# Kernel optimization log

Measured on AMD Instinct MI355X. Metric: run time of the kernel, lower is better.

The kernel has to match this reference:

```python
import jax, jax.numpy as jnp
import numpy as np

KH = KW = 3
K = KH * KW
GROUPS = 8


def conv_same(x, w, b=None):
    out = jax.lax.conv_general_dilated(x, w, (1, 1), 'SAME',
                                       dimension_numbers=('NHWC', 'HWIO', 'NHWC'))
    if b is not None:
        out = out + b
    return out


def feature_selection(x, w_att, w_sel):
    pooled = x.mean(axis=(1, 2), keepdims=True)            # [B,1,1,C]
    attn = jax.nn.sigmoid(conv_same(pooled, w_att))        # 1x1 conv, sigmoid
    return conv_same(x * (attn + 1.0), w_sel)              # [B,H,W,F]


def deform_sample(x, sy, sx):
    # x: [H,W,G,Cg]; sy,sx: [H,W,G,K] fractional sample coords (zero outside)
    H, W, G, _ = x.shape
    y0 = jnp.floor(sy)
    x0 = jnp.floor(sx)
    wy1 = sy - y0
    wx1 = sx - x0
    gi = jnp.arange(G)[None, None, :, None]

    def gather(yi, xi):
        valid = (yi >= 0) & (yi <= H - 1) & (xi >= 0) & (xi <= W - 1)
        yc = jnp.clip(yi, 0, H - 1).astype(jnp.int32)
        xc = jnp.clip(xi, 0, W - 1).astype(jnp.int32)
        v = x[yc, xc, gi]                                   # [H,W,G,K,Cg]
        return v * valid[..., None]

    v00 = gather(y0, x0)
    v01 = gather(y0, x0 + 1)
    v10 = gather(y0 + 1, x0)
    v11 = gather(y0 + 1, x0 + 1)
    wy1 = wy1[..., None]
    wx1 = wx1[..., None]
    top = v00 * (1 - wx1) + v01 * wx1
    bot = v10 * (1 - wx1) + v11 * wx1
    return top * (1 - wy1) + bot * wy1                      # [H,W,G,K,Cg]


def dcnv2(x, align, w_om, b_om, w_dcn, b_dcn):
    # x: [B,H,W,C] input to deform-conv; align: [B,H,W,Ca] alignment feature
    B, H, W, C = x.shape
    G = GROUPS
    Cg = C // G
    om = conv_same(align, w_om, b_om)                       # [B,H,W,G*3*K]
    off = om[..., :G * 2 * K].reshape(B, H, W, G, K, 2)     # (dy, dx)
    mask = jax.nn.sigmoid(om[..., G * 2 * K:]).reshape(B, H, W, G, K)

    iy = jnp.arange(H, dtype=x.dtype)[:, None, None, None]
    ix = jnp.arange(W, dtype=x.dtype)[None, :, None, None]
    ky, kx = jnp.meshgrid(jnp.arange(KH) - (KH - 1) // 2,
                          jnp.arange(KW) - (KW - 1) // 2, indexing='ij')
    ky = ky.reshape(K).astype(x.dtype)
    kx = kx.reshape(K).astype(x.dtype)
    sy = iy + ky + off[..., 0]                              # [B,H,W,G,K]
    sx = ix + kx + off[..., 1]

    xg = x.reshape(B, H, W, G, Cg)
    sampled = jax.vmap(deform_sample)(xg, sy, sx)           # [B,H,W,G,K,Cg]
    sampled = sampled * mask[..., None]
    sampled = sampled.transpose(0, 1, 2, 4, 3, 5).reshape(B, H, W, K, C)
    wk = w_dcn.reshape(K, C, -1)                            # [K,C,F]
    return jnp.einsum('bhwkc,kcf->bhwf', sampled, wk) + b_dcn


def reference(coarse, fine, w_att, w_sel, w_off, w_om, b_om, w_dcn, b_dcn):
    B, H, W, _ = fine.shape
    coarse_up = jax.image.resize(coarse, (B, H, W, coarse.shape[-1]), 'bilinear')
    fine_cal = feature_selection(fine, w_att, w_sel)
    fc = jnp.concatenate([fine_cal, coarse_up * 2.0], axis=-1)
    align = conv_same(fc, w_off)                            # 1x1, no bias
    aligned = jax.nn.relu(dcnv2(coarse_up, align, w_om, b_om, w_dcn, b_dcn))
    return aligned + fine_cal


def setup_inputs() -> dict:
    key = jax.random.key(0)
    ks = jax.random.split(key, 8)
    B, H, W = 4, 64, 64
    Cc, Cf, F = 256, 256, 256
    s = lambda fan: (2.0 / fan) ** 0.5
    return {
        'coarse': jax.random.normal(ks[0], (B, H // 2, W // 2, Cc), jnp.float32),
        'fine': jax.random.normal(ks[1], (B, H, W, Cf), jnp.float32),
        'w_att': jax.random.normal(ks[2], (1, 1, Cf, Cf), jnp.float32) * s(Cf),
        'w_sel': jax.random.normal(ks[3], (1, 1, Cf, F), jnp.float32) * s(Cf),
        'w_off': jax.random.normal(ks[4], (1, 1, F + Cc, 2 * F), jnp.float32) * s(F + Cc),
        'w_om': jax.random.normal(ks[5], (3, 3, 2 * F, GROUPS * 3 * K), jnp.float32) * 0.01,
        'b_om': jnp.zeros((GROUPS * 3 * K,), jnp.float32),
        'w_dcn': jax.random.normal(ks[6], (3, 3, Cc, F), jnp.float32) * s(9 * Cc),
        'b_dcn': jnp.zeros((F,), jnp.float32),
    }
```

## Files before the change

kernel.cpp:

```cpp
#include <hip/hip_runtime.h>
#include <hip/hip_bf16.h>
#include <cstddef>

constexpr int HWP = 64 * 64;
constexpr int CCH = 256;
constexpr int OMC = 216;
constexpr int KDC = 2304;

typedef __attribute__((ext_vector_type(8))) short bf16x8;
typedef __attribute__((ext_vector_type(4))) float f32x4;

__device__ inline unsigned short f2bf(float x) {
  __hip_bfloat16 h = __float2bfloat16(x);
  return *reinterpret_cast<unsigned short*>(&h);
}
__device__ inline float bf2f(unsigned short u) {
  unsigned int v = ((unsigned int)u) << 16;
  return __uint_as_float(v);
}
__device__ inline void bfpair(unsigned int u, float& a, float& b) {
  a = __uint_as_float(u << 16);
  b = __uint_as_float(u & 0xffff0000u);
}

__global__ __launch_bounds__(256) void prep_weights(
    const float* __restrict__ w_off, const float* __restrict__ w_om,
    const float* __restrict__ w_sel, const float* __restrict__ w_dcn,
    unsigned short* __restrict__ w_offT, unsigned short* __restrict__ w_omT,
    unsigned short* __restrict__ w_selT, unsigned short* __restrict__ w_dcnT) {
  int i = blockIdx.x * 256 + threadIdx.x;
  if (i < 512 * 512) {
    int n = i >> 9, k = i & 511;
    w_offT[i] = f2bf(w_off[k * 512 + n]);
  }
  if (i < 9 * 256 * 512) {
    int c = i & 511;
    int r = i >> 9;
    int tap = r >> 8;
    int n = r & 255;
    w_omT[i] = f2bf(n < OMC ? w_om[((size_t)tap * 512 + c) * OMC + n] : 0.f);
  }
  if (i < 256 * 256) {
    int n = i >> 8, k = i & 255;
    w_selT[i] = f2bf(w_sel[k * 256 + n]);
  }
  if (i < 9 * 256 * 256) {
    int tap = i >> 16, f = (i >> 8) & 255, c = i & 255;
    w_dcnT[i] = f2bf(w_dcn[((size_t)tap * 256 + c) * 256 + f]);
  }
}

__global__ __launch_bounds__(256) void pool_partial(
    const float* __restrict__ fine, float* __restrict__ partial) {
  int r = blockIdx.x;
  int b = blockIdx.y;
  int t = threadIdx.x;
  const float* src = fine + ((size_t)b * 4096 + r * 64) * 256 + t;
  float s = 0.f;
#pragma unroll 8
  for (int p = 0; p < 64; ++p) s += src[(size_t)p * 256];
  partial[((size_t)b * 64 + r) * 256 + t] = s;
}

__global__ __launch_bounds__(256) void pool_finish(
    const float* __restrict__ partial, const float* __restrict__ w_att,
    float* __restrict__ scale) {
  __shared__ float pl[256];
  int b = blockIdx.x;
  int t = threadIdx.x;
  const float* pp = partial + (size_t)b * 64 * 256 + t;
  float s = 0.f;
#pragma unroll 8
  for (int r = 0; r < 64; ++r) s += pp[(size_t)r * 256];
  pl[t] = s * (1.0f / 4096.0f);
  __syncthreads();
  float acc = 0.f;
  for (int ci = 0; ci < 256; ++ci) acc += pl[ci] * w_att[ci * 256 + t];
  scale[b * 256 + t] = 1.0f + 1.0f / (1.0f + expf(-acc));
}

__global__ __launch_bounds__(256) void upsample_kernel(
    const float* __restrict__ coarse, unsigned short* __restrict__ upbf,
    unsigned short* __restrict__ alignA) {
  int m = blockIdx.x;
  int c = threadIdx.x;
  int b = m >> 12, h = (m >> 6) & 63, w = m & 63;
  float cy = fminf(fmaxf(h * 0.5f - 0.25f, 0.f), 31.f);
  float cx = fminf(fmaxf(w * 0.5f - 0.25f, 0.f), 31.f);
  int y0 = (int)cy, x0 = (int)cx;
  float fy = cy - y0, fx = cx - x0;
  int y1 = min(y0 + 1, 31), x1 = min(x0 + 1, 31);
  const float* base = coarse + (size_t)b * 32 * 32 * CCH;
  float v00 = base[(y0 * 32 + x0) * CCH + c];
  float v01 = base[(y0 * 32 + x1) * CCH + c];
  float v10 = base[(y1 * 32 + x0) * CCH + c];
  float v11 = base[(y1 * 32 + x1) * CCH + c];
  float top = v00 + (v01 - v00) * fx;
  float bot = v10 + (v11 - v10) * fx;
  float v = top + (bot - top) * fy;
  upbf[(size_t)m * CCH + c] = f2bf(v);
  alignA[(size_t)m * 512 + 256 + c] = f2bf(2.f * v);
}

__global__ __launch_bounds__(256) void gemm_finecal_mfma(
    const float* __restrict__ fine, const float* __restrict__ scale,
    const unsigned short* __restrict__ w_selT,
    float* __restrict__ finecal, unsigned short* __restrict__ alignA) {
  __shared__ unsigned short As[128][72];
  __shared__ unsigned short Bs[64][72];
  __shared__ float sc[256];
  int n0 = blockIdx.x * 64;
  int m0 = blockIdx.y * 128;
  int t = threadIdx.x;
  int wid = t >> 6, lane = t & 63;
  int lrow = lane & 15, lq = lane >> 4;
  int bb = m0 >> 12;
  sc[t] = scale[bb * 256 + t];
  f32x4 acc[2][4];
#pragma unroll
  for (int i = 0; i < 2; ++i)
#pragma unroll
    for (int j = 0; j < 4; ++j) acc[i][j] = (f32x4){0.f, 0.f, 0.f, 0.f};
  for (int k0 = 0; k0 < 256; k0 += 64) {
    __syncthreads();
    for (int u = t; u < 128 * 8; u += 256) {
      int row = u >> 3, ck = u & 7;
      const float* fp = &fine[(size_t)(m0 + row) * 256 + k0 + ck * 8];
      float4 f0 = *(const float4*)fp;
      float4 f1 = *(const float4*)(fp + 4);
      int kb = k0 + ck * 8;
      ushort4 u0 = make_ushort4(f2bf(f0.x * sc[kb]), f2bf(f0.y * sc[kb + 1]),
                                f2bf(f0.z * sc[kb + 2]), f2bf(f0.w * sc[kb + 3]));
      ushort4 u1 = make_ushort4(f2bf(f1.x * sc[kb + 4]), f2bf(f1.y * sc[kb + 5]),
                                f2bf(f1.z * sc[kb + 6]), f2bf(f1.w * sc[kb + 7]));
      *(ushort4*)&As[row][ck * 8] = u0;
      *(ushort4*)&As[row][ck * 8 + 4] = u1;
    }
    for (int u = t; u < 64 * 8; u += 256) {
      int row = u >> 3, ck = u & 7;
      *(uint4*)&Bs[row][ck * 8] = *(const uint4*)&w_selT[(size_t)(n0 + row) * 256 + k0 + ck * 8];
    }
    __syncthreads();
#pragma unroll
    for (int kk = 0; kk < 2; ++kk) {
      bf16x8 a[2], b[4];
#pragma unroll
      for (int mt = 0; mt < 2; ++mt)
        a[mt] = *(const bf16x8*)&As[wid * 32 + mt * 16 + lrow][kk * 32 + lq * 8];
#pragma unroll
      for (int nt = 0; nt < 4; ++nt)
        b[nt] = *(const bf16x8*)&Bs[nt * 16 + lrow][kk * 32 + lq * 8];
#pragma unroll
      for (int mt = 0; mt < 2; ++mt)
#pragma unroll
        for (int nt = 0; nt < 4; ++nt)
          acc[mt][nt] = __builtin_amdgcn_mfma_f32_16x16x32_bf16(
              a[mt], b[nt], acc[mt][nt], 0, 0, 0);
    }
  }
#pragma unroll
  for (int mt = 0; mt < 2; ++mt)
#pragma unroll
    for (int nt = 0; nt < 4; ++nt)
#pragma unroll
      for (int r = 0; r < 4; ++r) {
        int m = m0 + wid * 32 + mt * 16 + lq * 4 + r;
        int n = n0 + nt * 16 + lrow;
        finecal[(size_t)m * 256 + n] = acc[mt][nt][r];
        alignA[(size_t)m * 512 + n] = f2bf(acc[mt][nt][r]);
      }
}

__global__ __launch_bounds__(256) void gemm_align_mfma(
    const unsigned short* __restrict__ alignA,
    const unsigned short* __restrict__ w_offT,
    unsigned short* __restrict__ alignBf) {
  __shared__ unsigned short As[128][72];
  __shared__ unsigned short Bs[64][72];
  int n0 = blockIdx.x * 64;
  int m0 = blockIdx.y * 128;
  int t = threadIdx.x;
  int wid = t >> 6, lane = t & 63;
  int lrow = lane & 15, lq = lane >> 4;
  f32x4 acc[2][4];
#pragma unroll
  for (int i = 0; i < 2; ++i)
#pragma unroll
    for (int j = 0; j < 4; ++j) acc[i][j] = (f32x4){0.f, 0.f, 0.f, 0.f};
  for (int k0 = 0; k0 < 512; k0 += 64) {
    __syncthreads();
    for (int u = t; u < 128 * 8; u += 256) {
      int row = u >> 3, ck = u & 7;
      *(uint4*)&As[row][ck * 8] =
          *(const uint4*)&alignA[(size_t)(m0 + row) * 512 + k0 + ck * 8];
    }
    for (int u = t; u < 64 * 8; u += 256) {
      int row = u >> 3, ck = u & 7;
      *(uint4*)&Bs[row][ck * 8] =
          *(const uint4*)&w_offT[(size_t)(n0 + row) * 512 + k0 + ck * 8];
    }
    __syncthreads();
#pragma unroll
    for (int kk = 0; kk < 2; ++kk) {
      bf16x8 a[2], b[4];
#pragma unroll
      for (int mt = 0; mt < 2; ++mt)
        a[mt] = *(const bf16x8*)&As[wid * 32 + mt * 16 + lrow][kk * 32 + lq * 8];
#pragma unroll
      for (int nt = 0; nt < 4; ++nt)
        b[nt] = *(const bf16x8*)&Bs[nt * 16 + lrow][kk * 32 + lq * 8];
#pragma unroll
      for (int mt = 0; mt < 2; ++mt)
#pragma unroll
        for (int nt = 0; nt < 4; ++nt)
          acc[mt][nt] = __builtin_amdgcn_mfma_f32_16x16x32_bf16(
              a[mt], b[nt], acc[mt][nt], 0, 0, 0);
    }
  }
#pragma unroll
  for (int mt = 0; mt < 2; ++mt)
#pragma unroll
    for (int nt = 0; nt < 4; ++nt)
#pragma unroll
      for (int r = 0; r < 4; ++r) {
        int m = m0 + wid * 32 + mt * 16 + lq * 4 + r;
        int n = n0 + nt * 16 + lrow;
        alignBf[(size_t)m * 512 + n] = f2bf(acc[mt][nt][r]);
      }
}

__global__ __launch_bounds__(256) void om_conv_mfma(
    const unsigned short* __restrict__ alignBf,
    const unsigned short* __restrict__ w_omT,
    const float* __restrict__ b_om,
    float* __restrict__ om) {
  __shared__ unsigned short As[4][66][72];
  __shared__ unsigned short Bs[2][64][72];
  int nblk = blockIdx.x;
  int mblk = blockIdx.y;
  int b = mblk >> 5, hp = mblk & 31;
  int h0 = hp * 2;
  int n0 = nblk * 64;
  int t = threadIdx.x;
  int wid = t >> 6, lane = t & 63;
  int wy = wid >> 1, wx = wid & 1;
  int lrow = lane & 15, lq = lane >> 4;
  const size_t imgbase = (size_t)b * 4096;
  f32x4 acc[4][2];
#pragma unroll
  for (int i = 0; i < 4; ++i)
#pragma unroll
    for (int j = 0; j < 2; ++j) acc[i][j] = (f32x4){0.f, 0.f, 0.f, 0.f};

  auto stageB = [&](int buf, int tap, int c0) {
    for (int u = t; u < 64 * 8; u += 256) {
      int n = u >> 3, ck = u & 7;
      *(uint4*)&Bs[buf][n][ck * 8] =
          *(const uint4*)&w_omT[((size_t)tap * 256 + n0 + n) * 512 + c0 * 64 + ck * 8];
    }
  };
  auto stageA = [&](int c0) {
    for (int u = t; u < 4 * 66 * 8; u += 256) {
      int dy = u / 528;
      int r = u - dy * 528;
      int px = r >> 3, ck = r & 7;
      int w = px - 1;
      int y = h0 - 1 + dy;
      uint4 v = make_uint4(0u, 0u, 0u, 0u);
      if (w >= 0 && w < 64 && y >= 0 && y < 64)
        v = *(const uint4*)&alignBf[(imgbase + y * 64 + w) * 512 + c0 * 64 + ck * 8];
      *(uint4*)&As[dy][px][ck * 8] = v;
    }
  };

  stageB(0, 0, 0);
  stageA(0);
  __syncthreads();
  int buf = 0;
  for (int c0 = 0; c0 < 8; ++c0) {
    for (int tap = 0; tap < 9; ++tap) {
      int ntap = tap + 1, nc0 = c0;
      if (ntap == 9) { ntap = 0; nc0 = (c0 + 1) & 7; }
      stageB(buf ^ 1, ntap, nc0);
      int dyt = tap / 3, dxt = tap - dyt * 3;
#pragma unroll
      for (int kk = 0; kk < 2; ++kk) {
        bf16x8 a[4], bb[2];
#pragma unroll
        for (int mt = 0; mt < 4; ++mt)
          a[mt] = *(const bf16x8*)&As[wy + dyt][mt * 16 + lrow + dxt][kk * 32 + lq * 8];
#pragma unroll
        for (int nt = 0; nt < 2; ++nt)
          bb[nt] = *(const bf16x8*)&Bs[buf][wx * 32 + nt * 16 + lrow][kk * 32 + lq * 8];
#pragma unroll
        for (int mt = 0; mt < 4; ++mt)
#pragma unroll
          for (int nt = 0; nt < 2; ++nt)
            acc[mt][nt] = __builtin_amdgcn_mfma_f32_16x16x32_bf16(
                a[mt], bb[nt], acc[mt][nt], 0, 0, 0);
      }
      __syncthreads();
      buf ^= 1;
    }
    if (c0 < 7) {
      stageA(c0 + 1);
      __syncthreads();
    }
  }
#pragma unroll
  for (int nt = 0; nt < 2; ++nt) {
    int n = n0 + wx * 32 + nt * 16 + lrow;
    if (n < OMC) {
      float bias = b_om[n];
#pragma unroll
      for (int mt = 0; mt < 4; ++mt) {
#pragma unroll
        for (int r = 0; r < 4; ++r) {
          size_t m = imgbase + (size_t)(h0 + wy) * 64 + mt * 16 + lq * 4 + r;
          om[m * OMC + n] = acc[mt][nt][r] + bias;
        }
      }
    }
  }
}

__global__ __launch_bounds__(256) void dcn_sample(
    const float* __restrict__ om, const unsigned short* __restrict__ upbf,
    unsigned short* __restrict__ S, int bh0) {
  __shared__ int offsA[256][4];
  __shared__ float wtsA[256][4];
  int blk = blockIdx.x;
  int bh = bh0 + (blk >> 1);
  int half = blk & 1;
  int b = bh >> 6, h = bh & 63;
  int p0 = half * 32;
  int m0g = bh * 64 + p0;
  int mloc0 = (bh - bh0) * 64 + p0;
  int t = threadIdx.x;
  const unsigned short* upb = upbf + (size_t)b * HWP * CCH;
  int lane = t & 63;
  int ph = t >> 6;
  int c = lane * 4;
  int g = lane >> 3;
  for (int tap = 0; tap < 9; ++tap) {
    int ky = tap / 3, kx = tap - ky * 3;
    __syncthreads();
    {
      int p = t >> 3, gg = t & 7;
      const float* omr = om + (size_t)(m0g + p) * OMC;
      float dy = omr[gg * 18 + tap * 2];
      float dx = omr[gg * 18 + tap * 2 + 1];
      float mk = 1.0f / (1.0f + expf(-omr[144 + gg * 9 + tap]));
      float sy = (float)(h + ky - 1) + dy;
      float sx = (float)(p0 + p + kx - 1) + dx;
      float y0f = floorf(sy), x0f = floorf(sx);
      float fy = sy - y0f, fx = sx - x0f;
      int y0 = (int)y0f, x0 = (int)x0f;
      int y1 = y0 + 1, x1 = x0 + 1;
      float vy0 = (y0 >= 0 && y0 <= 63) ? 1.f : 0.f;
      float vy1 = (y1 >= 0 && y1 <= 63) ? 1.f : 0.f;
      float vx0 = (x0 >= 0 && x0 <= 63) ? 1.f : 0.f;
      float vx1 = (x1 >= 0 && x1 <= 63) ? 1.f : 0.f;
      int yc0 = min(max(y0, 0), 63), yc1 = min(max(y1, 0), 63);
      int xc0 = min(max(x0, 0), 63), xc1 = min(max(x1, 0), 63);
      offsA[t][0] = (yc0 * 64 + xc0) * 256;
      offsA[t][1] = (yc0 * 64 + xc1) * 256;
      offsA[t][2] = (yc1 * 64 + xc0) * 256;
      offsA[t][3] = (yc1 * 64 + xc1) * 256;
      wtsA[t][0] = (1.f - fy) * (1.f - fx) * vy0 * vx0 * mk;
      wtsA[t][1] = (1.f - fy) * fx * vy0 * vx1 * mk;
      wtsA[t][2] = fy * (1.f - fx) * vy1 * vx0 * mk;
      wtsA[t][3] = fy * fx * vy1 * vx1 * mk;
    }
    __syncthreads();
#pragma unroll
    for (int pp = 0; pp < 8; ++pp) {
      int p = ph * 8 + pp;
      int idx = (p << 3) | g;
      int4 o = *(const int4*)&offsA[idx][0];
      float4 wv = *(const float4*)&wtsA[idx][0];
      uint2 u00 = *(const uint2*)&upb[o.x + c];
      uint2 u01 = *(const uint2*)&upb[o.y + c];
      uint2 u10 = *(const uint2*)&upb[o.z + c];
      uint2 u11 = *(const uint2*)&upb[o.w + c];
      float a0, a1, a2, a3, b0, b1, b2, b3, c0, c1, c2, c3, d0, d1, d2, d3;
      bfpair(u00.x, a0, a1); bfpair(u00.y, a2, a3);
      bfpair(u01.x, b0, b1); bfpair(u01.y, b2, b3);
      bfpair(u10.x, c0, c1); bfpair(u10.y, c2, c3);
      bfpair(u11.x, d0, d1); bfpair(u11.y, d2, d3);
      float v0 = wv.x * a0 + wv.y * b0 + wv.z * c0 + wv.w * d0;
      float v1 = wv.x * a1 + wv.y * b1 + wv.z * c1 + wv.w * d1;
      float v2 = wv.x * a2 + wv.y * b2 + wv.z * c2 + wv.w * d2;
      float v3 = wv.x * a3 + wv.y * b3 + wv.z * c3 + wv.w * d3;
      uint2 outv;
      outv.x = (unsigned int)f2bf(v0) | ((unsigned int)f2bf(v1) << 16);
      outv.y = (unsigned int)f2bf(v2) | ((unsigned int)f2bf(v3) << 16);
      *(uint2*)&S[(size_t)(mloc0 + p) * KDC + tap * 256 + c] = outv;
    }
  }
}

__global__ __launch_bounds__(256) void dcn_gemm(
    const unsigned short* __restrict__ S,
    const unsigned short* __restrict__ w_dcnT,
    const float* __restrict__ b_dcn,
    const float* __restrict__ finecal,
    float* __restrict__ outp, int m_base, int kiters) {
  __shared__ unsigned short As[2][128][72];
  __shared__ unsigned short Bs[2][128][72];
  int n0 = blockIdx.x * 128;
  int mloc0 = blockIdx.y * 128;
  int m0 = m_base + mloc0;
  int t = threadIdx.x;
  int wid = t >> 6, lane = t & 63;
  int wy = wid >> 1, wx = wid & 1;
  int lrow = lane & 15, lq = lane >> 4;
  f32x4 acc[4][4];
#pragma unroll
  for (int i = 0; i < 4; ++i)
#pragma unroll
    for (int j = 0; j < 4; ++j) acc[i][j] = (f32x4){0.f, 0.f, 0.f, 0.f};

  int arow = t >> 3, ack = t & 7;
  uint4 pa[4], pb[4];
  auto loadA = [&](int k0, uint4* p) {
#pragma unroll
    for (int i = 0; i < 4; ++i)
      p[i] = *(const uint4*)&S[(size_t)(mloc0 + arow + i * 32) * KDC + k0 + ack * 8];
  };
  auto loadB = [&](int k0, uint4* p) {
    int tap = k0 >> 8, c0 = k0 & 255;
#pragma unroll
    for (int i = 0; i < 4; ++i)
      p[i] = *(const uint4*)&w_dcnT[((size_t)tap * 256 + n0 + arow + i * 32) * 256 + c0 + ack * 8];
  };
  auto storeTiles = [&](int buf, const uint4* a, const uint4* b) {
#pragma unroll
    for (int i = 0; i < 4; ++i)
      *(uint4*)&As[buf][arow + i * 32][ack * 8] = a[i];
#pragma unroll
    for (int i = 0; i < 4; ++i)
      *(uint4*)&Bs[buf][arow + i * 32][ack * 8] = b[i];
  };

  loadA(0, pa);
  loadB(0, pb);
  storeTiles(0, pa, pb);
  __syncthreads();
  int buf = 0;
  for (int kb = 0; kb < kiters; ++kb) {
    bool has_next = (kb + 1) < kiters;
    if (has_next) {
      loadA((kb + 1) * 64, pa);
      loadB((kb + 1) * 64, pb);
    }
#pragma unroll
    for (int kk = 0; kk < 2; ++kk) {
      bf16x8 a[4], b[4];
#pragma unroll
      for (int mt = 0; mt < 4; ++mt)
        a[mt] = *(const bf16x8*)&As[buf][wy * 64 + mt * 16 + lrow][kk * 32 + lq * 8];
#pragma unroll
      for (int nt = 0; nt < 4; ++nt)
        b[nt] = *(const bf16x8*)&Bs[buf][wx * 64 + nt * 16 + lrow][kk * 32 + lq * 8];
#pragma unroll
      for (int mt = 0; mt < 4; ++mt)
#pragma unroll
        for (int nt = 0; nt < 4; ++nt)
          acc[mt][nt] = __builtin_amdgcn_mfma_f32_16x16x32_bf16(
              a[mt], b[nt], acc[mt][nt], 0, 0, 0);
    }
    if (has_next) {
      storeTiles(buf ^ 1, pa, pb);
      __syncthreads();
      buf ^= 1;
    }
  }
#pragma unroll
  for (int mt = 0; mt < 4; ++mt)
#pragma unroll
    for (int nt = 0; nt < 4; ++nt) {
      int f = n0 + wx * 64 + nt * 16 + lrow;
      float bias = b_dcn[f];
#pragma unroll
      for (int r = 0; r < 4; ++r) {
        int m = m0 + wy * 64 + mt * 16 + lq * 4 + r;
        float v = fmaxf(acc[mt][nt][r] + bias, 0.f);
        float fc = __builtin_nontemporal_load(&finecal[(size_t)m * 256 + f]);
        __builtin_nontemporal_store(v + fc, &outp[(size_t)m * 256 + f]);
      }
    }
}

extern "C" void kernel_launch(void* const* d_in, const int* in_sizes, int n_in,
                              void* d_out, int out_size, void* d_ws, size_t ws_size,
                              hipStream_t stream) {
  const float* coarse = (const float*)d_in[0];
  const float* fine   = (const float*)d_in[1];
  const float* w_att  = (const float*)d_in[2];
  const float* w_sel  = (const float*)d_in[3];
  const float* w_off  = (const float*)d_in[4];
  const float* w_om   = (const float*)d_in[5];
  const float* b_om   = (const float*)d_in[6];
  const float* w_dcn  = (const float*)d_in[7];
  const float* b_dcn  = (const float*)d_in[8];
  float* outp = (float*)d_out;

  char* base = (char*)d_ws;
  size_t o = 0;
  float* scale            = (float*)(base + o);          o += 4096;
  float* finecal          = (float*)(base + o);          o += 16777216;
  float* omb              = (float*)(base + o);          o += 14155776;
  unsigned short* upbf    = (unsigned short*)(base + o); o += 8388608;
  unsigned short* w_offT  = (unsigned short*)(base + o); o += 524288;
  unsigned short* w_omT   = (unsigned short*)(base + o); o += 2359296;
  unsigned short* w_selT  = (unsigned short*)(base + o); o += 131072;
  unsigned short* w_dcnT  = (unsigned short*)(base + o); o += 1179648;
  unsigned short* Sbuf    = (unsigned short*)(base + o);
  size_t fixed = o;
  unsigned short* alignA  = Sbuf;
  unsigned short* alignBf = (unsigned short*)((char*)Sbuf + 16777216);
  float* partial = omb;

  bool fullS = (ws_size >= fixed + 75497472);

  prep_weights<<<dim3(4608), dim3(256), 0, stream>>>(
      w_off, w_om, w_sel, w_dcn, w_offT, w_omT, w_selT, w_dcnT);
  pool_partial<<<dim3(64, 4), dim3(256), 0, stream>>>(fine, partial);
  pool_finish<<<dim3(4), dim3(256), 0, stream>>>(partial, w_att, scale);
  upsample_kernel<<<dim3(16384), dim3(256), 0, stream>>>(coarse, upbf, alignA);
  gemm_finecal_mfma<<<dim3(4, 128), dim3(256), 0, stream>>>(
      fine, scale, w_selT, finecal, alignA);
  gemm_align_mfma<<<dim3(8, 128), dim3(256), 0, stream>>>(alignA, w_offT, alignBf);
  om_conv_mfma<<<dim3(4, 128), dim3(256), 0, stream>>>(alignBf, w_omT, b_om, omb);

  if (fullS) {
    dcn_sample<<<dim3(512), dim3(256), 0, stream>>>(omb, upbf, Sbuf, 0);
    dcn_gemm<<<dim3(2, 128), dim3(256), 0, stream>>>(
        Sbuf, w_dcnT, b_dcn, finecal, outp, 0, KDC / 64);
  } else {
    for (int ch = 0; ch < 2; ++ch) {
      dcn_sample<<<dim3(256), dim3(256), 0, stream>>>(omb, upbf, Sbuf, ch * 128);
      dcn_gemm<<<dim3(2, 64), dim3(256), 0, stream>>>(
          Sbuf, w_dcnT, b_dcn, finecal, outp, ch * 8192, KDC / 64);
    }
  }
}
```

Before: 424.0 us.

## Widen om_conv N tile to 128 and prefetch weights through registers

The offset/mask 3x3 conv kernel now computes 128 output channels per block instead of 64. That halves the grid and halves how often each block re-stages the same input tile from alignBf. Weight tiles for the next tap are loaded into registers before the MFMA work and written to shared memory afterwards, so global load latency overlaps compute. The cost is more accumulator registers and LDS per block, a smaller grid that may occupy the GPU less fully, and wasted MFMAs on padded channels beyond 216.

Result: slower. 451.3 us (+6.4%).

```diff
diff --git a/kernel.cpp b/kernel.cpp
--- a/kernel.cpp
+++ b/kernel.cpp
@@ -235,29 +235,35 @@
     const float* __restrict__ b_om,
     float* __restrict__ om) {
   __shared__ unsigned short As[4][66][72];
-  __shared__ unsigned short Bs[2][64][72];
+  __shared__ unsigned short Bs[2][128][72];
   int nblk = blockIdx.x;
   int mblk = blockIdx.y;
   int b = mblk >> 5, hp = mblk & 31;
   int h0 = hp * 2;
-  int n0 = nblk * 64;
+  int n0 = nblk * 128;
   int t = threadIdx.x;
   int wid = t >> 6, lane = t & 63;
   int wy = wid >> 1, wx = wid & 1;
   int lrow = lane & 15, lq = lane >> 4;
   const size_t imgbase = (size_t)b * 4096;
-  f32x4 acc[4][2];
+  f32x4 acc[4][4];
 #pragma unroll
   for (int i = 0; i < 4; ++i)
 #pragma unroll
-    for (int j = 0; j < 2; ++j) acc[i][j] = (f32x4){0.f, 0.f, 0.f, 0.f};
-
-  auto stageB = [&](int buf, int tap, int c0) {
-    for (int u = t; u < 64 * 8; u += 256) {
-      int n = u >> 3, ck = u & 7;
-      *(uint4*)&Bs[buf][n][ck * 8] =
-          *(const uint4*)&w_omT[((size_t)tap * 256 + n0 + n) * 512 + c0 * 64 + ck * 8];
-    }
+    for (int j = 0; j < 4; ++j) acc[i][j] = (f32x4){0.f, 0.f, 0.f, 0.f};
+
+  int brow = t >> 3, bck = t & 7;
+  uint4 pb[4];
+  auto loadB = [&](int tap, int c0, uint4* p) {
+#pragma unroll
+    for (int i = 0; i < 4; ++i)
+      p[i] = *(const uint4*)&w_omT[((size_t)tap * 256 + n0 + brow + i * 32) * 512 +
+                                   c0 * 64 + bck * 8];
+  };
+  auto storeB = [&](int buf, const uint4* p) {
+#pragma unroll
+    for (int i = 0; i < 4; ++i)
+      *(uint4*)&Bs[buf][brow + i * 32][bck * 8] = p[i];
   };
   auto stageA = [&](int c0) {
     for (int u = t; u < 4 * 66 * 8; u += 256) {
@@ -273,43 +279,48 @@
     }
   };
 
-  stageB(0, 0, 0);
+  loadB(0, 0, pb);
+  storeB(0, pb);
   stageA(0);
   __syncthreads();
   int buf = 0;
   for (int c0 = 0; c0 < 8; ++c0) {
     for (int tap = 0; tap < 9; ++tap) {
       int ntap = tap + 1, nc0 = c0;
-      if (ntap == 9) { ntap = 0; nc0 = (c0 + 1) & 7; }
-      stageB(buf ^ 1, ntap, nc0);
+      bool has_next = true;
+      if (ntap == 9) { ntap = 0; nc0 = c0 + 1; has_next = (nc0 < 8); }
+      if (has_next) loadB(ntap, nc0, pb);
       int dyt = tap / 3, dxt = tap - dyt * 3;
 #pragma unroll
       for (int kk = 0; kk < 2; ++kk) {
-        bf16x8 a[4], bb[2];
+        bf16x8 a[4], bb[4];
 #pragma unroll
         for (int mt = 0; mt < 4; ++mt)
           a[mt] = *(const bf16x8*)&As[wy + dyt][mt * 16 + lrow + dxt][kk * 32 + lq * 8];
 #pragma unroll
-        for (int nt = 0; nt < 2; ++nt)
-          bb[nt] = *(const bf16x8*)&Bs[buf][wx * 32 + nt * 16 + lrow][kk * 32 + lq * 8];
+        for (int nt = 0; nt < 4; ++nt)
+          bb[nt] = *(const bf16x8*)&Bs[buf][wx * 64 + nt * 16 + lrow][kk * 32 + lq * 8];
 #pragma unroll
         for (int mt = 0; mt < 4; ++mt)
 #pragma unroll
-          for (int nt = 0; nt < 2; ++nt)
+          for (int nt = 0; nt < 4; ++nt)
             acc[mt][nt] = __builtin_amdgcn_mfma_f32_16x16x32_bf16(
                 a[mt], bb[nt], acc[mt][nt], 0, 0, 0);
       }
-      __syncthreads();
-      buf ^= 1;
-    }
-    if (c0 < 7) {
-      stageA(c0 + 1);
-      __syncthreads();
-    }
-  }
-#pragma unroll
-  for (int nt = 0; nt < 2; ++nt) {
-    int n = n0 + wx * 32 + nt * 16 + lrow;
+      if (has_next) {
+        storeB(buf ^ 1, pb);
+        __syncthreads();
+        buf ^= 1;
+        if (tap == 8) {
+          stageA(nc0);
+          __syncthreads();
+        }
+      }
+    }
+  }
+#pragma unroll
+  for (int nt = 0; nt < 4; ++nt) {
+    int n = n0 + wx * 64 + nt * 16 + lrow;
     if (n < OMC) {
       float bias = b_om[n];
 #pragma unroll
@@ -532,7 +543,7 @@
   gemm_finecal_mfma<<<dim3(4, 128), dim3(256), 0, stream>>>(
       fine, scale, w_selT, finecal, alignA);
   gemm_align_mfma<<<dim3(8, 128), dim3(256), 0, stream>>>(alignA, w_offT, alignBf);
-  om_conv_mfma<<<dim3(4, 128), dim3(256), 0, stream>>>(alignBf, w_omT, b_om, omb);
+  om_conv_mfma<<<dim3(2, 128), dim3(256), 0, stream>>>(alignBf, w_omT, b_om, omb);
 
   if (fullS) {
     dcn_sample<<<dim3(512), dim3(256), 0, stream>>>(omb, upbf, Sbuf, 0);
```
